# Kernel optimization log

Measured on AMD Instinct MI355X. Metric: run time of the kernel, lower is better.

## Reference

```python
import jax, jax.numpy as jnp
import numpy as np

N_NODES = 50000
N_EDGES = 1600000
IN_CH = 128
OUT_CH = 64
N_HEADS = 4


def setup_inputs() -> dict:
    key = jax.random.key(0)
    k1, k2, k3, k4, k5 = jax.random.split(key, 5)
    x_source = jax.random.normal(k1, (N_NODES, IN_CH), dtype=jnp.float32)
    edge_tgt = jax.random.randint(k2, (N_EDGES,), 0, N_NODES, dtype=jnp.int32)
    edge_src = jax.random.randint(k3, (N_EDGES,), 0, N_NODES, dtype=jnp.int32)
    edge_vals = jnp.ones((N_EDGES,), dtype=jnp.float32)
    # per-head learned params (xavier_uniform-ish scale)
    w_scale = float(np.sqrt(6.0 / (IN_CH + OUT_CH)))
    weight = jax.random.uniform(k4, (N_HEADS, IN_CH, OUT_CH), dtype=jnp.float32,
                                minval=-w_scale, maxval=w_scale)
    a_scale = float(np.sqrt(6.0 / (2 * OUT_CH)))
    att_weight = jax.random.uniform(k5, (N_HEADS, 2 * OUT_CH), dtype=jnp.float32,
                                    minval=-a_scale, maxval=a_scale)
    return {"x_source": x_source, "edge_tgt": edge_tgt, "edge_src": edge_src,
            "edge_vals": edge_vals, "weight": weight, "att_weight": att_weight}


def _can_forward(x_source, edge_tgt, edge_src, edge_vals, weight, att_weight):
    n_nodes = x_source.shape[0]
    out_ch = weight.shape[-1]
    # per-head linear transform: [N, H, O]
    x_msg = jnp.einsum('ni,hio->nho', x_source, weight)
    # gather per-edge source/target messages: [E, H, O]
    src_msg = x_msg[edge_src]
    tgt_msg = x_msg[edge_tgt]
    # attention score = cat([src, tgt]) @ att_weight, split halves: [E, H]
    aw_s = att_weight[:, :out_ch]
    aw_t = att_weight[:, out_ch:]
    e = jnp.einsum('eho,ho->eh', src_msg, aw_s) + jnp.einsum('eho,ho->eh', tgt_msg, aw_t)
    e = jax.nn.leaky_relu(e, negative_slope=0.01)  # default torch slope
    e = e * edge_vals[:, None]  # multiply by neighborhood values pre-softmax
    # sparse softmax over each target row (dim=1 of the sparse matrix)
    row_max = jax.ops.segment_max(e, edge_tgt, num_segments=n_nodes)  # [N, H]
    e_exp = jnp.exp(e - row_max[edge_tgt])
    row_sum = jax.ops.segment_sum(e_exp, edge_tgt, num_segments=n_nodes)  # [N, H]
    alpha = e_exp / row_sum[edge_tgt]  # [E, H]
    # weighted aggregate of source messages per target node: [N, H, O]
    out = jax.ops.segment_sum(alpha[:, :, None] * src_msg, edge_tgt,
                              num_segments=n_nodes)
    # concat heads -> [N, H*O]
    return out.reshape(n_nodes, -1)


def reference(x_source, edge_tgt, edge_src, edge_vals, weight, att_weight):
    return _can_forward(x_source, edge_tgt, edge_src, edge_vals, weight, att_weight)
```

## Files before the change

kernel.cpp:

```cpp
#include <hip/hip_runtime.h>
#include <hip/hip_bf16.h>
#include <math.h>

#define N_NODES 50000
#define N_EDGES 1600000
#define IN_CH   128
#define OUT_CH  64
#define N_HEADS 4
#define CH      (N_HEADS * OUT_CH)

#define NPB   64
#define BINS  782
#define CAPB  3072
#define CHUNK 8000

typedef __attribute__((ext_vector_type(8))) short bf16x8;
typedef __attribute__((ext_vector_type(4))) float f32x4;

__device__ __forceinline__ float bf16_lo(unsigned u) { return __uint_as_float(u << 16); }
__device__ __forceinline__ float bf16_hi(unsigned u) { return __uint_as_float(u & 0xffff0000u); }
__device__ __forceinline__ unsigned short f_to_bf16(float f) {
  unsigned u = __float_as_uint(f);
  u += 0x7fffu + ((u >> 16) & 1u);
  return (unsigned short)(u >> 16);
}

__global__ __launch_bounds__(256) void convert_w(
    const float* __restrict__ w, unsigned short* __restrict__ wb)
{
  int i = blockIdx.x * 256 + threadIdx.x;
  if (i >= N_HEADS * IN_CH * OUT_CH) return;
  int j = i & 7, lane = (i >> 3) & 63, ctg = (i >> 9) & 15, kc = i >> 13;
  int k = kc * 32 + (lane >> 4) * 8 + j;
  int n = ctg * 16 + (lane & 15);
  int h = n >> 6, o = n & 63;
  wb[i] = f_to_bf16(w[(h * IN_CH + k) * OUT_CH + o]);
}

__global__ __launch_bounds__(256) void init_cursors(int* __restrict__ gcur)
{
  int b = blockIdx.x * 256 + threadIdx.x;
  if (b < BINS) gcur[b] = b * CAPB;
}

__global__ __launch_bounds__(256) void gemm_mfma(
    const float* __restrict__ x, const unsigned short* __restrict__ wb,
    const float* __restrict__ aw,
    unsigned short* __restrict__ xmsg, float* __restrict__ sbuf, float* __restrict__ tbuf)
{
  __shared__ __align__(16) unsigned short tlds[4][32][128];

  const int lane = threadIdx.x & 63;
  const int wv   = threadIdx.x >> 6;
  const int q    = lane >> 4;
  const int l16  = lane & 15;
  const int rowbase = blockIdx.x * 64 + (wv >> 1) * 32;
  const int chalf   = wv & 1;

  bf16x8 afrag[2][4];
  #pragma unroll
  for (int s = 0; s < 2; ++s) {
    int r = rowbase + s * 16 + l16;
    r = min(r, N_NODES - 1);
    const float* xp = x + (size_t)r * IN_CH + q * 8;
    #pragma unroll
    for (int kc = 0; kc < 4; ++kc) {
      f32x4 lo = *(const f32x4*)(xp + kc * 32);
      f32x4 hi = *(const f32x4*)(xp + kc * 32 + 4);
      bf16x8 a;
      a[0] = (short)f_to_bf16(lo[0]); a[1] = (short)f_to_bf16(lo[1]);
      a[2] = (short)f_to_bf16(lo[2]); a[3] = (short)f_to_bf16(lo[3]);
      a[4] = (short)f_to_bf16(hi[0]); a[5] = (short)f_to_bf16(hi[1]);
      a[6] = (short)f_to_bf16(hi[2]); a[7] = (short)f_to_bf16(hi[3]);
      afrag[s][kc] = a;
    }
  }

  f32x4 acc[2][8];
  #pragma unroll
  for (int s = 0; s < 2; ++s)
    #pragma unroll
    for (int ct = 0; ct < 8; ++ct)
      acc[s][ct] = (f32x4){0.f, 0.f, 0.f, 0.f};

  #pragma unroll
  for (int kc = 0; kc < 4; ++kc) {
    #pragma unroll
    for (int ct = 0; ct < 8; ++ct) {
      const int ctg = chalf * 8 + ct;
      bf16x8 b = *(const bf16x8*)(wb + ((size_t)(kc * 16 + ctg) * 64 + lane) * 8);
      acc[0][ct] = __builtin_amdgcn_mfma_f32_16x16x32_bf16(afrag[0][kc], b, acc[0][ct], 0, 0, 0);
      acc[1][ct] = __builtin_amdgcn_mfma_f32_16x16x32_bf16(afrag[1][kc], b, acc[1][ct], 0, 0, 0);
    }
  }

  #pragma unroll
  for (int s = 0; s < 2; ++s)
    #pragma unroll
    for (int ct = 0; ct < 8; ++ct)
      #pragma unroll
      for (int reg = 0; reg < 4; ++reg)
        tlds[wv][s * 16 + q * 4 + reg][ct * 16 + l16] = f_to_bf16(acc[s][ct][reg]);

  #pragma unroll
  for (int s = 0; s < 2; ++s) {
    float ps[2][4] = {{0,0,0,0},{0,0,0,0}};
    float pt[2][4] = {{0,0,0,0},{0,0,0,0}};
    #pragma unroll
    for (int ct = 0; ct < 8; ++ct) {
      int col = chalf * 128 + ct * 16 + l16;
      int h = col >> 6;
      float as_ = aw[h * 128 + (col & 63)];
      float at_ = aw[h * 128 + 64 + (col & 63)];
      int hp = ct >> 2;
      #pragma unroll
      for (int reg = 0; reg < 4; ++reg) {
        float v = acc[s][ct][reg];
        ps[hp][reg] += v * as_;
        pt[hp][reg] += v * at_;
      }
    }
    #pragma unroll
    for (int hp = 0; hp < 2; ++hp)
      #pragma unroll
      for (int reg = 0; reg < 4; ++reg)
        #pragma unroll
        for (int off = 1; off < 16; off <<= 1) {
          ps[hp][reg] += __shfl_xor(ps[hp][reg], off);
          pt[hp][reg] += __shfl_xor(pt[hp][reg], off);
        }
    const int rowq = rowbase + s * 16 + q * 4;
    if (l16 == 0) {
      #pragma unroll
      for (int reg = 0; reg < 4; ++reg) {
        int r = rowq + reg;
        if (r < N_NODES) {
          #pragma unroll
          for (int hp = 0; hp < 2; ++hp) {
            sbuf[r * 4 + chalf * 2 + hp] = ps[hp][reg];
            tbuf[r * 4 + chalf * 2 + hp] = pt[hp][reg];
          }
        }
      }
    }
  }

  __syncthreads();

  const int seg  = lane & 31;
  const int half = lane >> 5;
  #pragma unroll
  for (int r2 = 0; r2 < 16; ++r2) {
    int row = r2 * 2 + half;
    int gr = rowbase + row;
    if (gr < N_NODES) {
      ushort4 vv = *(const ushort4*)&tlds[wv][row][seg * 4];
      *(ushort4*)(xmsg + (size_t)gr * CH + chalf * 128 + seg * 4) = vv;
    }
  }
}

__global__ __launch_bounds__(256) void bin_scatter(
    const int* __restrict__ etgt, const int* __restrict__ esrc,
    const float* __restrict__ eval, int* __restrict__ gcur, int2* __restrict__ binned)
{
  __shared__ int lhist[BINS];
  __shared__ int lbase[BINS];
  __shared__ unsigned short stg[CHUNK];

  const int tid = threadIdx.x;
  const int e0 = blockIdx.x * CHUNK;
  const int n = min(CHUNK, N_EDGES - e0);

  for (int b = tid; b < BINS; b += 256) lhist[b] = 0;
  __syncthreads();

  for (int i = tid; i < n; i += 256) {
    int t = etgt[e0 + i];
    stg[i] = (unsigned short)t;
    atomicAdd(&lhist[t >> 6], 1);
  }
  __syncthreads();

  for (int b = tid; b < BINS; b += 256) {
    int c = lhist[b];
    lbase[b] = c ? atomicAdd(&gcur[b], c) : 0;
    lhist[b] = 0;
  }
  __syncthreads();

  for (int i = tid; i < n; i += 256) {
    int t = (int)stg[i];
    int b = t >> 6;
    int r = atomicAdd(&lhist[b], 1);
    int pos = lbase[b] + r;
    if (pos < (b + 1) * CAPB) {
      int pack = esrc[e0 + i] | ((t & 63) << 16);
      binned[pos] = make_int2(pack, __float_as_int(eval[e0 + i]));
    }
  }
}

__global__ __launch_bounds__(256) void build_csr(
    const int* __restrict__ gcur, const int2* __restrict__ binned,
    int2* __restrict__ csr, int* __restrict__ deg, int* __restrict__ rowstart)
{
  __shared__ int nh[NPB];
  __shared__ int npre[NPB];
  __shared__ __align__(16) int2 stg[CAPB];

  const int tid = threadIdx.x;
  const int b = blockIdx.x;
  const int base = b * CAPB;
  const int cnt = min(gcur[b] - base, CAPB);

  if (tid < NPB) nh[tid] = 0;
  __syncthreads();

  for (int i = tid; i < cnt; i += 256) {
    int2 e = binned[base + i];
    stg[i] = e;
    atomicAdd(&nh[(e.x >> 16) & 63], 1);
  }
  __syncthreads();

  if (tid < 64) {
    int v = nh[tid];
    int sc = v;
    #pragma unroll
    for (int off = 1; off < 64; off <<= 1) {
      int u = __shfl_up(sc, off);
      if (tid >= off) sc += u;
    }
    npre[tid] = sc - v;
    int node = b * NPB + tid;
    if (node < N_NODES) { deg[node] = v; rowstart[node] = base + sc - v; }
    nh[tid] = 0;
  }
  __syncthreads();

  for (int i = tid; i < cnt; i += 256) {
    int2 e = stg[i];
    int tl = (e.x >> 16) & 63;
    int r = atomicAdd(&nh[tl], 1);
    csr[base + npre[tl] + r] = e;
  }
}

__global__ __launch_bounds__(256) void aggregate_kernel(
    const int* __restrict__ deg, const int* __restrict__ rowstart,
    const int2* __restrict__ csr,
    const float* __restrict__ sbuf, const float* __restrict__ tbuf,
    const unsigned short* __restrict__ xmsg, float* __restrict__ out)
{
  const int lane = threadIdx.x & 63;
  const int wave = threadIdx.x >> 6;
  const int n = blockIdx.x * 4 + wave;
  if (n >= N_NODES) return;

  __shared__ __align__(16) float p_lds[4][64][4];
  __shared__ int s_lds[4][64];

  const int d = deg[n];
  const int rs0 = rowstart[n];
  const int seg  = lane & 31;
  const int half = lane >> 5;
  const int hh4  = seg >> 3;

  float4 tn4 = *(const float4*)(tbuf + (size_t)n * 4);
  float tn[4] = {tn4.x, tn4.y, tn4.z, tn4.w};

  float m[4]    = {-INFINITY, -INFINITY, -INFINITY, -INFINITY};
  float psum[4] = {0.f, 0.f, 0.f, 0.f};
  float acc[8]  = {0.f, 0.f, 0.f, 0.f, 0.f, 0.f, 0.f, 0.f};

  for (int base = 0; base < d; base += 64) {
    const int cnt = min(64, d - base);
    const bool act = lane < cnt;

    float sc[4] = {-INFINITY, -INFINITY, -INFINITY, -INFINITY};
    int s = 0;
    if (act) {
      int2 ev = csr[(size_t)rs0 + base + lane];
      s = ev.x & 0xffff;
      float v = __int_as_float(ev.y);
      float4 sv4 = *(const float4*)(sbuf + (size_t)s * 4);
      float svv[4] = {sv4.x, sv4.y, sv4.z, sv4.w};
      #pragma unroll
      for (int hh = 0; hh < 4; ++hh) {
        float t = svv[hh] + tn[hh];
        t = (t > 0.f) ? t : 0.01f * t;
        sc[hh] = t * v;
      }
    }

    float bm[4] = {sc[0], sc[1], sc[2], sc[3]};
    #pragma unroll
    for (int hh = 0; hh < 4; ++hh)
      #pragma unroll
      for (int off = 32; off; off >>= 1)
        bm[hh] = fmaxf(bm[hh], __shfl_xor(bm[hh], off));

    float p[4];
    #pragma unroll
    for (int hh = 0; hh < 4; ++hh) {
      float nm = fmaxf(m[hh], bm[hh]);
      float r = (m[hh] == -INFINITY) ? 0.f : __expf(m[hh] - nm);
      psum[hh] *= r;
      if (hh == hh4) {
        #pragma unroll
        for (int j = 0; j < 8; ++j) acc[j] *= r;
      }
      m[hh] = nm;
      p[hh] = act ? __expf(sc[hh] - nm) : 0.f;
      psum[hh] += p[hh];
    }

    if (act) {
      s_lds[wave][lane] = s;
      *(float4*)(&p_lds[wave][lane][0]) = make_float4(p[0], p[1], p[2], p[3]);
    }
    __builtin_amdgcn_wave_barrier();

    int k = 0;
    for (; k + 8 <= cnt; k += 8) {
      int sA = s_lds[wave][k + 0 + half];
      int sB = s_lds[wave][k + 2 + half];
      int sC = s_lds[wave][k + 4 + half];
      int sD = s_lds[wave][k + 6 + half];
      uint4 rA = *(const uint4*)(xmsg + (size_t)sA * CH + seg * 8);
      uint4 rB = *(const uint4*)(xmsg + (size_t)sB * CH + seg * 8);
      uint4 rC = *(const uint4*)(xmsg + (size_t)sC * CH + seg * 8);
      uint4 rD = *(const uint4*)(xmsg + (size_t)sD * CH + seg * 8);
      float qA = p_lds[wave][k + 0 + half][hh4];
      float qB = p_lds[wave][k + 2 + half][hh4];
      float qC = p_lds[wave][k + 4 + half][hh4];
      float qD = p_lds[wave][k + 6 + half][hh4];
      acc[0] = fmaf(qA, bf16_lo(rA.x), acc[0]); acc[1] = fmaf(qA, bf16_hi(rA.x), acc[1]);
      acc[2] = fmaf(qA, bf16_lo(rA.y), acc[2]); acc[3] = fmaf(qA, bf16_hi(rA.y), acc[3]);
      acc[4] = fmaf(qA, bf16_lo(rA.z), acc[4]); acc[5] = fmaf(qA, bf16_hi(rA.z), acc[5]);
      acc[6] = fmaf(qA, bf16_lo(rA.w), acc[6]); acc[7] = fmaf(qA, bf16_hi(rA.w), acc[7]);
      acc[0] = fmaf(qB, bf16_lo(rB.x), acc[0]); acc[1] = fmaf(qB, bf16_hi(rB.x), acc[1]);
      acc[2] = fmaf(qB, bf16_lo(rB.y), acc[2]); acc[3] = fmaf(qB, bf16_hi(rB.y), acc[3]);
      acc[4] = fmaf(qB, bf16_lo(rB.z), acc[4]); acc[5] = fmaf(qB, bf16_hi(rB.z), acc[5]);
      acc[6] = fmaf(qB, bf16_lo(rB.w), acc[6]); acc[7] = fmaf(qB, bf16_hi(rB.w), acc[7]);
      acc[0] = fmaf(qC, bf16_lo(rC.x), acc[0]); acc[1] = fmaf(qC, bf16_hi(rC.x), acc[1]);
      acc[2] = fmaf(qC, bf16_lo(rC.y), acc[2]); acc[3] = fmaf(qC, bf16_hi(rC.y), acc[3]);
      acc[4] = fmaf(qC, bf16_lo(rC.z), acc[4]); acc[5] = fmaf(qC, bf16_hi(rC.z), acc[5]);
      acc[6] = fmaf(qC, bf16_lo(rC.w), acc[6]); acc[7] = fmaf(qC, bf16_hi(rC.w), acc[7]);
      acc[0] = fmaf(qD, bf16_lo(rD.x), acc[0]); acc[1] = fmaf(qD, bf16_hi(rD.x), acc[1]);
      acc[2] = fmaf(qD, bf16_lo(rD.y), acc[2]); acc[3] = fmaf(qD, bf16_hi(rD.y), acc[3]);
      acc[4] = fmaf(qD, bf16_lo(rD.z), acc[4]); acc[5] = fmaf(qD, bf16_hi(rD.z), acc[5]);
      acc[6] = fmaf(qD, bf16_lo(rD.w), acc[6]); acc[7] = fmaf(qD, bf16_hi(rD.w), acc[7]);
    }
    for (; k < cnt; k += 2) {
      int e = k + half;
      if (e < cnt) {
        int sA = s_lds[wave][e];
        uint4 rA = *(const uint4*)(xmsg + (size_t)sA * CH + seg * 8);
        float qA = p_lds[wave][e][hh4];
        acc[0] = fmaf(qA, bf16_lo(rA.x), acc[0]); acc[1] = fmaf(qA, bf16_hi(rA.x), acc[1]);
        acc[2] = fmaf(qA, bf16_lo(rA.y), acc[2]); acc[3] = fmaf(qA, bf16_hi(rA.y), acc[3]);
        acc[4] = fmaf(qA, bf16_lo(rA.z), acc[4]); acc[5] = fmaf(qA, bf16_hi(rA.z), acc[5]);
        acc[6] = fmaf(qA, bf16_lo(rA.w), acc[6]); acc[7] = fmaf(qA, bf16_hi(rA.w), acc[7]);
      }
    }
    __builtin_amdgcn_wave_barrier();
  }

  #pragma unroll
  for (int j = 0; j < 8; ++j) acc[j] += __shfl_xor(acc[j], 32);
  #pragma unroll
  for (int hh = 0; hh < 4; ++hh)
    #pragma unroll
    for (int off = 32; off; off >>= 1)
      psum[hh] += __shfl_xor(psum[hh], off);

  float rs = psum[hh4];
  float inv = (rs > 0.f) ? 1.0f / rs : 0.f;
  const int o = half * 4;
  float4 o4 = make_float4(acc[o+0]*inv, acc[o+1]*inv, acc[o+2]*inv, acc[o+3]*inv);
  *(float4*)(out + (size_t)n * CH + seg * 8 + half * 4) = o4;
}

extern "C" void kernel_launch(void* const* d_in, const int* in_sizes, int n_in,
                              void* d_out, int out_size, void* d_ws, size_t ws_size,
                              hipStream_t stream) {
  const float* x    = (const float*)d_in[0];
  const int*   etgt = (const int*)  d_in[1];
  const int*   esrc = (const int*)  d_in[2];
  const float* evl  = (const float*)d_in[3];
  const float* w    = (const float*)d_in[4];
  const float* aw   = (const float*)d_in[5];
  float* out = (float*)d_out;

  char* ws = (char*)d_ws;
  unsigned short* wb   = (unsigned short*)(ws);
  unsigned short* xmsg = (unsigned short*)(ws + 65536);
  float* sbuf     = (float*)(ws + 25665536);
  float* tbuf     = (float*)(ws + 26465536);
  int*   gcur     = (int*)  (ws + 27265536);
  int*   deg      = (int*)  (ws + 27269632);
  int*   rowstart = (int*)  (ws + 27470336);
  int2*  binned   = (int2*) (ws + 27671040);
  int2*  csr      = (int2*) (ws + 46889472);

  init_cursors<<<4, 256, 0, stream>>>(gcur);
  convert_w<<<128, 256, 0, stream>>>(w, wb);
  gemm_mfma<<<(N_NODES + 63) / 64, 256, 0, stream>>>(x, wb, aw, xmsg, sbuf, tbuf);
  bin_scatter<<<(N_EDGES + CHUNK - 1) / CHUNK, 256, 0, stream>>>(etgt, esrc, evl, gcur, binned);
  build_csr<<<BINS, 256, 0, stream>>>(gcur, binned, csr, deg, rowstart);
  aggregate_kernel<<<(N_NODES + 3) / 4, 256, 0, stream>>>(deg, rowstart, csr,
                                                          sbuf, tbuf, xmsg, out);
}
```

Baseline: 288.5 us.

## Merge prep kernels, transpose GEMM tiling, and aggregate two nodes per wave

Merges weight conversion and cursor init into one prep kernel. Swaps the MFMA operand roles so each wave computes all 256 output channels for 32 nodes, which removes the LDS transpose staging and the 16-lane shuffle reductions. The aggregation kernel now handles two target nodes per wave, interleaving their gathers to expose more memory-level parallelism. In exchange it uses more registers, may lower occupancy, and leaves work imbalanced when the two nodes have different degrees.

```diff
diff --git a/kernel.cpp b/kernel.cpp
--- a/kernel.cpp
+++ b/kernel.cpp
@@ -25,137 +25,103 @@
   return (unsigned short)(u >> 16);
 }
 
-__global__ __launch_bounds__(256) void convert_w(
-    const float* __restrict__ w, unsigned short* __restrict__ wb)
+__global__ __launch_bounds__(256) void prep_kernel(
+    const float* __restrict__ w, unsigned short* __restrict__ wb2,
+    int* __restrict__ gcur)
 {
-  int i = blockIdx.x * 256 + threadIdx.x;
-  if (i >= N_HEADS * IN_CH * OUT_CH) return;
-  int j = i & 7, lane = (i >> 3) & 63, ctg = (i >> 9) & 15, kc = i >> 13;
-  int k = kc * 32 + (lane >> 4) * 8 + j;
-  int n = ctg * 16 + (lane & 15);
-  int h = n >> 6, o = n & 63;
-  wb[i] = f_to_bf16(w[(h * IN_CH + k) * OUT_CH + o]);
-}
-
-__global__ __launch_bounds__(256) void init_cursors(int* __restrict__ gcur)
-{
-  int b = blockIdx.x * 256 + threadIdx.x;
-  if (b < BINS) gcur[b] = b * CAPB;
+  if (blockIdx.x < 128) {
+    int i = blockIdx.x * 256 + threadIdx.x;
+    int j = i & 7, lane = (i >> 3) & 63, kc = (i >> 9) & 3, mb = i >> 11;
+    int k = kc * 32 + (lane >> 4) * 8 + j;
+    int ch = mb * 16 + (lane & 15);
+    int h = ch >> 6, o = ch & 63;
+    wb2[i] = f_to_bf16(w[(h * IN_CH + k) * OUT_CH + o]);
+  } else {
+    for (int b = threadIdx.x; b < BINS; b += 256) gcur[b] = b * CAPB;
+  }
 }
 
 __global__ __launch_bounds__(256) void gemm_mfma(
-    const float* __restrict__ x, const unsigned short* __restrict__ wb,
+    const float* __restrict__ x, const unsigned short* __restrict__ wb2,
     const float* __restrict__ aw,
     unsigned short* __restrict__ xmsg, float* __restrict__ sbuf, float* __restrict__ tbuf)
 {
-  __shared__ __align__(16) unsigned short tlds[4][32][128];
-
   const int lane = threadIdx.x & 63;
   const int wv   = threadIdx.x >> 6;
   const int q    = lane >> 4;
   const int l16  = lane & 15;
-  const int rowbase = blockIdx.x * 64 + (wv >> 1) * 32;
-  const int chalf   = wv & 1;
-
-  bf16x8 afrag[2][4];
-  #pragma unroll
-  for (int s = 0; s < 2; ++s) {
-    int r = rowbase + s * 16 + l16;
-    r = min(r, N_NODES - 1);
-    const float* xp = x + (size_t)r * IN_CH + q * 8;
+  const int nb   = blockIdx.x * 128 + wv * 32;
+
+  bf16x8 bfrag[2][4];
+  #pragma unroll
+  for (int t = 0; t < 2; ++t) {
+    int node = min(nb + t * 16 + l16, N_NODES - 1);
+    const float* xp = x + (size_t)node * IN_CH + q * 8;
     #pragma unroll
     for (int kc = 0; kc < 4; ++kc) {
       f32x4 lo = *(const f32x4*)(xp + kc * 32);
       f32x4 hi = *(const f32x4*)(xp + kc * 32 + 4);
-      bf16x8 a;
-      a[0] = (short)f_to_bf16(lo[0]); a[1] = (short)f_to_bf16(lo[1]);
-      a[2] = (short)f_to_bf16(lo[2]); a[3] = (short)f_to_bf16(lo[3]);
-      a[4] = (short)f_to_bf16(hi[0]); a[5] = (short)f_to_bf16(hi[1]);
-      a[6] = (short)f_to_bf16(hi[2]); a[7] = (short)f_to_bf16(hi[3]);
-      afrag[s][kc] = a;
-    }
-  }
-
-  f32x4 acc[2][8];
-  #pragma unroll
-  for (int s = 0; s < 2; ++s)
-    #pragma unroll
-    for (int ct = 0; ct < 8; ++ct)
-      acc[s][ct] = (f32x4){0.f, 0.f, 0.f, 0.f};
+      bf16x8 b;
+      b[0] = (short)f_to_bf16(lo[0]); b[1] = (short)f_to_bf16(lo[1]);
+      b[2] = (short)f_to_bf16(lo[2]); b[3] = (short)f_to_bf16(lo[3]);
+      b[4] = (short)f_to_bf16(hi[0]); b[5] = (short)f_to_bf16(hi[1]);
+      b[6] = (short)f_to_bf16(hi[2]); b[7] = (short)f_to_bf16(hi[3]);
+      bfrag[t][kc] = b;
+    }
+  }
+
+  f32x4 acc[2][16];
+  #pragma unroll
+  for (int t = 0; t < 2; ++t)
+    #pragma unroll
+    for (int mb = 0; mb < 16; ++mb)
+      acc[t][mb] = (f32x4){0.f, 0.f, 0.f, 0.f};
 
   #pragma unroll
   for (int kc = 0; kc < 4; ++kc) {
     #pragma unroll
-    for (int ct = 0; ct < 8; ++ct) {
-      const int ctg = chalf * 8 + ct;
-      bf16x8 b = *(const bf16x8*)(wb + ((size_t)(kc * 16 + ctg) * 64 + lane) * 8);
-      acc[0][ct] = __builtin_amdgcn_mfma_f32_16x16x32_bf16(afrag[0][kc], b, acc[0][ct], 0, 0, 0);
-      acc[1][ct] = __builtin_amdgcn_mfma_f32_16x16x32_bf16(afrag[1][kc], b, acc[1][ct], 0, 0, 0);
-    }
-  }
-
-  #pragma unroll
-  for (int s = 0; s < 2; ++s)
-    #pragma unroll
-    for (int ct = 0; ct < 8; ++ct)
-      #pragma unroll
-      for (int reg = 0; reg < 4; ++reg)
-        tlds[wv][s * 16 + q * 4 + reg][ct * 16 + l16] = f_to_bf16(acc[s][ct][reg]);
-
-  #pragma unroll
-  for (int s = 0; s < 2; ++s) {
-    float ps[2][4] = {{0,0,0,0},{0,0,0,0}};
-    float pt[2][4] = {{0,0,0,0},{0,0,0,0}};
-    #pragma unroll
-    for (int ct = 0; ct < 8; ++ct) {
-      int col = chalf * 128 + ct * 16 + l16;
-      int h = col >> 6;
-      float as_ = aw[h * 128 + (col & 63)];
-      float at_ = aw[h * 128 + 64 + (col & 63)];
-      int hp = ct >> 2;
+    for (int mb = 0; mb < 16; ++mb) {
+      bf16x8 a = *(const bf16x8*)(wb2 + ((size_t)(mb * 4 + kc) * 64 + lane) * 8);
+      acc[0][mb] = __builtin_amdgcn_mfma_f32_16x16x32_bf16(a, bfrag[0][kc], acc[0][mb], 0, 0, 0);
+      acc[1][mb] = __builtin_amdgcn_mfma_f32_16x16x32_bf16(a, bfrag[1][kc], acc[1][mb], 0, 0, 0);
+    }
+  }
+
+  #pragma unroll
+  for (int t = 0; t < 2; ++t) {
+    const int node = nb + t * 16 + l16;
+    const bool valid = node < N_NODES;
+
+    float sv[4] = {0.f, 0.f, 0.f, 0.f};
+    float tv[4] = {0.f, 0.f, 0.f, 0.f};
+    #pragma unroll
+    for (int mb = 0; mb < 16; ++mb) {
+      ushort4 pk;
+      pk.x = f_to_bf16(acc[t][mb][0]); pk.y = f_to_bf16(acc[t][mb][1]);
+      pk.z = f_to_bf16(acc[t][mb][2]); pk.w = f_to_bf16(acc[t][mb][3]);
+      if (valid)
+        *(ushort4*)(xmsg + (size_t)node * CH + mb * 16 + q * 4) = pk;
+
+      const int h = mb >> 2;
+      const int o = (mb & 3) * 16 + q * 4;
       #pragma unroll
       for (int reg = 0; reg < 4; ++reg) {
-        float v = acc[s][ct][reg];
-        ps[hp][reg] += v * as_;
-        pt[hp][reg] += v * at_;
-      }
-    }
-    #pragma unroll
-    for (int hp = 0; hp < 2; ++hp)
-      #pragma unroll
-      for (int reg = 0; reg < 4; ++reg)
-        #pragma unroll
-        for (int off = 1; off < 16; off <<= 1) {
-          ps[hp][reg] += __shfl_xor(ps[hp][reg], off);
-          pt[hp][reg] += __shfl_xor(pt[hp][reg], off);
-        }
-    const int rowq = rowbase + s * 16 + q * 4;
-    if (l16 == 0) {
-      #pragma unroll
-      for (int reg = 0; reg < 4; ++reg) {
-        int r = rowq + reg;
-        if (r < N_NODES) {
-          #pragma unroll
-          for (int hp = 0; hp < 2; ++hp) {
-            sbuf[r * 4 + chalf * 2 + hp] = ps[hp][reg];
-            tbuf[r * 4 + chalf * 2 + hp] = pt[hp][reg];
-          }
-        }
-      }
-    }
-  }
-
-  __syncthreads();
-
-  const int seg  = lane & 31;
-  const int half = lane >> 5;
-  #pragma unroll
-  for (int r2 = 0; r2 < 16; ++r2) {
-    int row = r2 * 2 + half;
-    int gr = rowbase + row;
-    if (gr < N_NODES) {
-      ushort4 vv = *(const ushort4*)&tlds[wv][row][seg * 4];
-      *(ushort4*)(xmsg + (size_t)gr * CH + chalf * 128 + seg * 4) = vv;
+        float as_ = aw[h * 128 + o + reg];
+        float at_ = aw[h * 128 + 64 + o + reg];
+        sv[h] += acc[t][mb][reg] * as_;
+        tv[h] += acc[t][mb][reg] * at_;
+      }
+    }
+    #pragma unroll
+    for (int hh = 0; hh < 4; ++hh) {
+      sv[hh] += __shfl_xor(sv[hh], 16); sv[hh] += __shfl_xor(sv[hh], 32);
+      tv[hh] += __shfl_xor(tv[hh], 16); tv[hh] += __shfl_xor(tv[hh], 32);
+    }
+    float svq = (q == 0) ? sv[0] : (q == 1) ? sv[1] : (q == 2) ? sv[2] : sv[3];
+    float tvq = (q == 0) ? tv[0] : (q == 1) ? tv[1] : (q == 2) ? tv[2] : tv[3];
+    if (valid) {
+      sbuf[node * 4 + q] = svq;
+      tbuf[node * 4 + q] = tvq;
     }
   }
 }
@@ -255,132 +221,196 @@
 {
   const int lane = threadIdx.x & 63;
   const int wave = threadIdx.x >> 6;
-  const int n = blockIdx.x * 4 + wave;
-  if (n >= N_NODES) return;
-
-  __shared__ __align__(16) float p_lds[4][64][4];
-  __shared__ int s_lds[4][64];
-
-  const int d = deg[n];
-  const int rs0 = rowstart[n];
+  const int n0 = (blockIdx.x * 4 + wave) * 2;
+  const int n1 = n0 + 1;
+
+  __shared__ __align__(16) float p_lds[4][2][64][4];
+  __shared__ int s_lds[4][2][64];
+
   const int seg  = lane & 31;
   const int half = lane >> 5;
   const int hh4  = seg >> 3;
 
-  float4 tn4 = *(const float4*)(tbuf + (size_t)n * 4);
-  float tn[4] = {tn4.x, tn4.y, tn4.z, tn4.w};
-
-  float m[4]    = {-INFINITY, -INFINITY, -INFINITY, -INFINITY};
-  float psum[4] = {0.f, 0.f, 0.f, 0.f};
-  float acc[8]  = {0.f, 0.f, 0.f, 0.f, 0.f, 0.f, 0.f, 0.f};
-
-  for (int base = 0; base < d; base += 64) {
-    const int cnt = min(64, d - base);
-    const bool act = lane < cnt;
-
-    float sc[4] = {-INFINITY, -INFINITY, -INFINITY, -INFINITY};
-    int s = 0;
-    if (act) {
-      int2 ev = csr[(size_t)rs0 + base + lane];
-      s = ev.x & 0xffff;
-      float v = __int_as_float(ev.y);
-      float4 sv4 = *(const float4*)(sbuf + (size_t)s * 4);
-      float svv[4] = {sv4.x, sv4.y, sv4.z, sv4.w};
+  const int d0 = deg[n0], r0 = rowstart[n0];
+  const int d1 = deg[n1], r1 = rowstart[n1];
+
+  float4 t04 = *(const float4*)(tbuf + (size_t)n0 * 4);
+  float4 t14 = *(const float4*)(tbuf + (size_t)n1 * 4);
+  float tn0[4] = {t04.x, t04.y, t04.z, t04.w};
+  float tn1[4] = {t14.x, t14.y, t14.z, t14.w};
+
+  float m0[4] = {-INFINITY, -INFINITY, -INFINITY, -INFINITY};
+  float m1[4] = {-INFINITY, -INFINITY, -INFINITY, -INFINITY};
+  float ps0[4] = {0.f, 0.f, 0.f, 0.f};
+  float ps1[4] = {0.f, 0.f, 0.f, 0.f};
+  float acc0[8] = {0.f, 0.f, 0.f, 0.f, 0.f, 0.f, 0.f, 0.f};
+  float acc1[8] = {0.f, 0.f, 0.f, 0.f, 0.f, 0.f, 0.f, 0.f};
+
+  const int dmax = max(d0, d1);
+  for (int base = 0; base < dmax; base += 64) {
+    const int cnt0 = min(64, d0 - base);
+    const int cnt1 = min(64, d1 - base);
+    const bool any0 = cnt0 > 0, any1 = cnt1 > 0;
+    const bool act0 = lane < cnt0, act1 = lane < cnt1;
+
+    int2 ev0, ev1;
+    if (act0) ev0 = csr[(size_t)r0 + base + lane];
+    if (act1) ev1 = csr[(size_t)r1 + base + lane];
+    int s0 = 0, s1 = 0;
+    float4 sv40, sv41;
+    if (act0) { s0 = ev0.x & 0xffff; sv40 = *(const float4*)(sbuf + (size_t)s0 * 4); }
+    if (act1) { s1 = ev1.x & 0xffff; sv41 = *(const float4*)(sbuf + (size_t)s1 * 4); }
+
+    float sc0[4] = {-INFINITY, -INFINITY, -INFINITY, -INFINITY};
+    float sc1[4] = {-INFINITY, -INFINITY, -INFINITY, -INFINITY};
+    if (act0) {
+      float v = __int_as_float(ev0.y);
+      float sw[4] = {sv40.x, sv40.y, sv40.z, sv40.w};
       #pragma unroll
       for (int hh = 0; hh < 4; ++hh) {
-        float t = svv[hh] + tn[hh];
+        float t = sw[hh] + tn0[hh];
         t = (t > 0.f) ? t : 0.01f * t;
-        sc[hh] = t * v;
-      }
-    }
-
-    float bm[4] = {sc[0], sc[1], sc[2], sc[3]};
+        sc0[hh] = t * v;
+      }
+    }
+    if (act1) {
+      float v = __int_as_float(ev1.y);
+      float sw[4] = {sv41.x, sv41.y, sv41.z, sv41.w};
+      #pragma unroll
+      for (int hh = 0; hh < 4; ++hh) {
+        float t = sw[hh] + tn1[hh];
+        t = (t > 0.f) ? t : 0.01f * t;
+        sc1[hh] = t * v;
+      }
+    }
+
+    float bm0[4] = {sc0[0], sc0[1], sc0[2], sc0[3]};
+    float bm1[4] = {sc1[0], sc1[1], sc1[2], sc1[3]};
     #pragma unroll
     for (int hh = 0; hh < 4; ++hh)
       #pragma unroll
-      for (int off = 32; off; off >>= 1)
-        bm[hh] = fmaxf(bm[hh], __shfl_xor(bm[hh], off));
-
-    float p[4];
-    #pragma unroll
-    for (int hh = 0; hh < 4; ++hh) {
-      float nm = fmaxf(m[hh], bm[hh]);
-      float r = (m[hh] == -INFINITY) ? 0.f : __expf(m[hh] - nm);
-      psum[hh] *= r;
-      if (hh == hh4) {
+      for (int off = 32; off; off >>= 1) {
+        bm0[hh] = fmaxf(bm0[hh], __shfl_xor(bm0[hh], off));
+        bm1[hh] = fmaxf(bm1[hh], __shfl_xor(bm1[hh], off));
+      }
+
+    if (any0) {
+      float p[4];
+      #pragma unroll
+      for (int hh = 0; hh < 4; ++hh) {
+        float nm = fmaxf(m0[hh], bm0[hh]);
+        float r = (m0[hh] == -INFINITY) ? 0.f : __expf(m0[hh] - nm);
+        ps0[hh] *= r;
+        if (hh == hh4) {
+          #pragma unroll
+          for (int j = 0; j < 8; ++j) acc0[j] *= r;
+        }
+        m0[hh] = nm;
+        p[hh] = act0 ? __expf(sc0[hh] - nm) : 0.f;
+        ps0[hh] += p[hh];
+      }
+      if (act0) {
+        s_lds[wave][0][lane] = s0;
+        *(float4*)(&p_lds[wave][0][lane][0]) = make_float4(p[0], p[1], p[2], p[3]);
+      }
+    }
+    if (any1) {
+      float p[4];
+      #pragma unroll
+      for (int hh = 0; hh < 4; ++hh) {
+        float nm = fmaxf(m1[hh], bm1[hh]);
+        float r = (m1[hh] == -INFINITY) ? 0.f : __expf(m1[hh] - nm);
+        ps1[hh] *= r;
+        if (hh == hh4) {
+          #pragma unroll
+          for (int j = 0; j < 8; ++j) acc1[j] *= r;
+        }
+        m1[hh] = nm;
+        p[hh] = act1 ? __expf(sc1[hh] - nm) : 0.f;
+        ps1[hh] += p[hh];
+      }
+      if (act1) {
+        s_lds[wave][1][lane] = s1;
+        *(float4*)(&p_lds[wave][1][lane][0]) = make_float4(p[0], p[1], p[2], p[3]);
+      }
+    }
+    __builtin_amdgcn_wave_barrier();
+
+    const int kmax = max(max(cnt0, cnt1), 0);
+    for (int k = 0; k < kmax; k += 8) {
+      const bool g0 = k < cnt0, g1 = k < cnt1;
+      uint4 R0[4], R1[4];
+      float Q0[4], Q1[4];
+      if (g0) {
+        const int c = cnt0 - 1;
         #pragma unroll
-        for (int j = 0; j < 8; ++j) acc[j] *= r;
-      }
-      m[hh] = nm;
-      p[hh] = act ? __expf(sc[hh] - nm) : 0.f;
-      psum[hh] += p[hh];
-    }
-
-    if (act) {
-      s_lds[wave][lane] = s;
-      *(float4*)(&p_lds[wave][lane][0]) = make_float4(p[0], p[1], p[2], p[3]);
+        for (int i = 0; i < 4; ++i) {
+          int ii = k + 2 * i + half;
+          int j = min(ii, c);
+          R0[i] = *(const uint4*)(xmsg + (size_t)s_lds[wave][0][j] * CH + seg * 8);
+          Q0[i] = (ii < cnt0) ? p_lds[wave][0][j][hh4] : 0.f;
+        }
+      }
+      if (g1) {
+        const int c = cnt1 - 1;
+        #pragma unroll
+        for (int i = 0; i < 4; ++i) {
+          int ii = k + 2 * i + half;
+          int j = min(ii, c);
+          R1[i] = *(const uint4*)(xmsg + (size_t)s_lds[wave][1][j] * CH + seg * 8);
+          Q1[i] = (ii < cnt1) ? p_lds[wave][1][j][hh4] : 0.f;
+        }
+      }
+      if (g0) {
+        #pragma unroll
+        for (int i = 0; i < 4; ++i) {
+          float qq = Q0[i]; uint4 rr = R0[i];
+          acc0[0] = fmaf(qq, bf16_lo(rr.x), acc0[0]); acc0[1] = fmaf(qq, bf16_hi(rr.x), acc0[1]);
+          acc0[2] = fmaf(qq, bf16_lo(rr.y), acc0[2]); acc0[3] = fmaf(qq, bf16_hi(rr.y), acc0[3]);
+          acc0[4] = fmaf(qq, bf16_lo(rr.z), acc0[4]); acc0[5] = fmaf(qq, bf16_hi(rr.z), acc0[5]);
+          acc0[6] = fmaf(qq, bf16_lo(rr.w), acc0[6]); acc0[7] = fmaf(qq, bf16_hi(rr.w), acc0[7]);
+        }
+      }
+      if (g1) {
+        #pragma unroll
+        for (int i = 0; i < 4; ++i) {
+          float qq = Q1[i]; uint4 rr = R1[i];
+          acc1[0] = fmaf(qq, bf16_lo(rr.x), acc1[0]); acc1[1] = fmaf(qq, bf16_hi(rr.x), acc1[1]);
+          acc1[2] = fmaf(qq, bf16_lo(rr.y), acc1[2]); acc1[3] = fmaf(qq, bf16_hi(rr.y), acc1[3]);
+          acc1[4] = fmaf(qq, bf16_lo(rr.z), acc1[4]); acc1[5] = fmaf(qq, bf16_hi(rr.z), acc1[5]);
+          acc1[6] = fmaf(qq, bf16_lo(rr.w), acc1[6]); acc1[7] = fmaf(qq, bf16_hi(rr.w), acc1[7]);
+        }
+      }
     }
     __builtin_amdgcn_wave_barrier();
-
-    int k = 0;
-    for (; k + 8 <= cnt; k += 8) {
-      int sA = s_lds[wave][k + 0 + half];
-      int sB = s_lds[wave][k + 2 + half];
-      int sC = s_lds[wave][k + 4 + half];
-      int sD = s_lds[wave][k + 6 + half];
-      uint4 rA = *(const uint4*)(xmsg + (size_t)sA * CH + seg * 8);
-      uint4 rB = *(const uint4*)(xmsg + (size_t)sB * CH + seg * 8);
-      uint4 rC = *(const uint4*)(xmsg + (size_t)sC * CH + seg * 8);
-      uint4 rD = *(const uint4*)(xmsg + (size_t)sD * CH + seg * 8);
-      float qA = p_lds[wave][k + 0 + half][hh4];
-      float qB = p_lds[wave][k + 2 + half][hh4];
-      float qC = p_lds[wave][k + 4 + half][hh4];
-      float qD = p_lds[wave][k + 6 + half][hh4];
-      acc[0] = fmaf(qA, bf16_lo(rA.x), acc[0]); acc[1] = fmaf(qA, bf16_hi(rA.x), acc[1]);
-      acc[2] = fmaf(qA, bf16_lo(rA.y), acc[2]); acc[3] = fmaf(qA, bf16_hi(rA.y), acc[3]);
-      acc[4] = fmaf(qA, bf16_lo(rA.z), acc[4]); acc[5] = fmaf(qA, bf16_hi(rA.z), acc[5]);
-      acc[6] = fmaf(qA, bf16_lo(rA.w), acc[6]); acc[7] = fmaf(qA, bf16_hi(rA.w), acc[7]);
-      acc[0] = fmaf(qB, bf16_lo(rB.x), acc[0]); acc[1] = fmaf(qB, bf16_hi(rB.x), acc[1]);
-      acc[2] = fmaf(qB, bf16_lo(rB.y), acc[2]); acc[3] = fmaf(qB, bf16_hi(rB.y), acc[3]);
-      acc[4] = fmaf(qB, bf16_lo(rB.z), acc[4]); acc[5] = fmaf(qB, bf16_hi(rB.z), acc[5]);
-      acc[6] = fmaf(qB, bf16_lo(rB.w), acc[6]); acc[7] = fmaf(qB, bf16_hi(rB.w), acc[7]);
-      acc[0] = fmaf(qC, bf16_lo(rC.x), acc[0]); acc[1] = fmaf(qC, bf16_hi(rC.x), acc[1]);
-      acc[2] = fmaf(qC, bf16_lo(rC.y), acc[2]); acc[3] = fmaf(qC, bf16_hi(rC.y), acc[3]);
-      acc[4] = fmaf(qC, bf16_lo(rC.z), acc[4]); acc[5] = fmaf(qC, bf16_hi(rC.z), acc[5]);
-      acc[6] = fmaf(qC, bf16_lo(rC.w), acc[6]); acc[7] = fmaf(qC, bf16_hi(rC.w), acc[7]);
-      acc[0] = fmaf(qD, bf16_lo(rD.x), acc[0]); acc[1] = fmaf(qD, bf16_hi(rD.x), acc[1]);
-      acc[2] = fmaf(qD, bf16_lo(rD.y), acc[2]); acc[3] = fmaf(qD, bf16_hi(rD.y), acc[3]);
-      acc[4] = fmaf(qD, bf16_lo(rD.z), acc[4]); acc[5] = fmaf(qD, bf16_hi(rD.z), acc[5]);
-      acc[6] = fmaf(qD, bf16_lo(rD.w), acc[6]); acc[7] = fmaf(qD, bf16_hi(rD.w), acc[7]);
-    }
-    for (; k < cnt; k += 2) {
-      int e = k + half;
-      if (e < cnt) {
-        int sA = s_lds[wave][e];
-        uint4 rA = *(const uint4*)(xmsg + (size_t)sA * CH + seg * 8);
-        float qA = p_lds[wave][e][hh4];
-        acc[0] = fmaf(qA, bf16_lo(rA.x), acc[0]); acc[1] = fmaf(qA, bf16_hi(rA.x), acc[1]);
-        acc[2] = fmaf(qA, bf16_lo(rA.y), acc[2]); acc[3] = fmaf(qA, bf16_hi(rA.y), acc[3]);
-        acc[4] = fmaf(qA, bf16_lo(rA.z), acc[4]); acc[5] = fmaf(qA, bf16_hi(rA.z), acc[5]);
-        acc[6] = fmaf(qA, bf16_lo(rA.w), acc[6]); acc[7] = fmaf(qA, bf16_hi(rA.w), acc[7]);
-      }
-    }
-    __builtin_amdgcn_wave_barrier();
-  }
-
-  #pragma unroll
-  for (int j = 0; j < 8; ++j) acc[j] += __shfl_xor(acc[j], 32);
+  }
+
+  #pragma unroll
+  for (int j = 0; j < 8; ++j) {
+    acc0[j] += __shfl_xor(acc0[j], 32);
+    acc1[j] += __shfl_xor(acc1[j], 32);
+  }
   #pragma unroll
   for (int hh = 0; hh < 4; ++hh)
     #pragma unroll
-    for (int off = 32; off; off >>= 1)
-      psum[hh] += __shfl_xor(psum[hh], off);
-
-  float rs = psum[hh4];
-  float inv = (rs > 0.f) ? 1.0f / rs : 0.f;
+    for (int off = 32; off; off >>= 1) {
+      ps0[hh] += __shfl_xor(ps0[hh], off);
+      ps1[hh] += __shfl_xor(ps1[hh], off);
+    }
+
   const int o = half * 4;
-  float4 o4 = make_float4(acc[o+0]*inv, acc[o+1]*inv, acc[o+2]*inv, acc[o+3]*inv);
-  *(float4*)(out + (size_t)n * CH + seg * 8 + half * 4) = o4;
+  {
+    float rs = ps0[hh4];
+    float inv = (rs > 0.f) ? 1.0f / rs : 0.f;
+    float4 o4 = make_float4(acc0[o+0]*inv, acc0[o+1]*inv, acc0[o+2]*inv, acc0[o+3]*inv);
+    *(float4*)(out + (size_t)n0 * CH + seg * 8 + o) = o4;
+  }
+  {
+    float rs = ps1[hh4];
+    float inv = (rs > 0.f) ? 1.0f / rs : 0.f;
+    float4 o4 = make_float4(acc1[o+0]*inv, acc1[o+1]*inv, acc1[o+2]*inv, acc1[o+3]*inv);
+    *(float4*)(out + (size_t)n1 * CH + seg * 8 + o) = o4;
+  }
 }
 
 extern "C" void kernel_launch(void* const* d_in, const int* in_sizes, int n_in,
@@ -395,7 +425,7 @@
   float* out = (float*)d_out;
 
   char* ws = (char*)d_ws;
-  unsigned short* wb   = (unsigned short*)(ws);
+  unsigned short* wb2  = (unsigned short*)(ws);
   unsigned short* xmsg = (unsigned short*)(ws + 65536);
   float* sbuf     = (float*)(ws + 25665536);
   float* tbuf     = (float*)(ws + 26465536);
@@ -405,11 +435,10 @@
   int2*  binned   = (int2*) (ws + 27671040);
   int2*  csr      = (int2*) (ws + 46889472);
 
-  init_cursors<<<4, 256, 0, stream>>>(gcur);
-  convert_w<<<128, 256, 0, stream>>>(w, wb);
-  gemm_mfma<<<(N_NODES + 63) / 64, 256, 0, stream>>>(x, wb, aw, xmsg, sbuf, tbuf);
+  prep_kernel<<<129, 256, 0, stream>>>(w, wb2, gcur);
+  gemm_mfma<<<(N_NODES + 127) / 128, 256, 0, stream>>>(x, wb2, aw, xmsg, sbuf, tbuf);
   bin_scatter<<<(N_EDGES + CHUNK - 1) / CHUNK, 256, 0, stream>>>(etgt, esrc, evl, gcur, binned);
   build_csr<<<BINS, 256, 0, stream>>>(gcur, binned, csr, deg, rowstart);
-  aggregate_kernel<<<(N_NODES + 3) / 4, 256, 0, stream>>>(deg, rowstart, csr,
-                                                          sbuf, tbuf, xmsg, out);
-}
+  aggregate_kernel<<<N_NODES / 8, 256, 0, stream>>>(deg, rowstart, csr,
+                                                    sbuf, tbuf, xmsg, out);
+}
```

Result: no change. 293.5 us (+1.7%).

## Switch messages to fp16, use packed half FMA aggregation, restructure GEMM, merge prep kernels

Applied to the files above, without the earlier changes.

Stores the transformed messages in fp16 instead of bf16 and accumulates the weighted aggregation with packed half2 FMAs, which roughly halves the FMA count in the gather loop. The GEMM is rewritten with a transposed MFMA layout: each wave covers 32 nodes across all 256 channels and writes xmsg directly without the LDS staging buffer or block sync. The weight conversion and cursor init kernels are merged into one launch, and the bin_scatter chunk size is halved to launch more blocks. Accumulating in half precision risks precision loss and overflow on high-degree nodes.

```diff
diff --git a/kernel.cpp b/kernel.cpp
--- a/kernel.cpp
+++ b/kernel.cpp
@@ -1,5 +1,6 @@
 #include <hip/hip_runtime.h>
 #include <hip/hip_bf16.h>
+#include <hip/hip_fp16.h>
 #include <math.h>
 
 #define N_NODES 50000
@@ -12,150 +13,114 @@
 #define NPB   64
 #define BINS  782
 #define CAPB  3072
-#define CHUNK 8000
-
-typedef __attribute__((ext_vector_type(8))) short bf16x8;
+#define CHUNK 4000
+
+typedef __attribute__((ext_vector_type(8))) _Float16 f16x8;
 typedef __attribute__((ext_vector_type(4))) float f32x4;
 
-__device__ __forceinline__ float bf16_lo(unsigned u) { return __uint_as_float(u << 16); }
-__device__ __forceinline__ float bf16_hi(unsigned u) { return __uint_as_float(u & 0xffff0000u); }
-__device__ __forceinline__ unsigned short f_to_bf16(float f) {
-  unsigned u = __float_as_uint(f);
-  u += 0x7fffu + ((u >> 16) & 1u);
-  return (unsigned short)(u >> 16);
-}
-
-__global__ __launch_bounds__(256) void convert_w(
-    const float* __restrict__ w, unsigned short* __restrict__ wb)
-{
-  int i = blockIdx.x * 256 + threadIdx.x;
-  if (i >= N_HEADS * IN_CH * OUT_CH) return;
-  int j = i & 7, lane = (i >> 3) & 63, ctg = (i >> 9) & 15, kc = i >> 13;
-  int k = kc * 32 + (lane >> 4) * 8 + j;
-  int n = ctg * 16 + (lane & 15);
-  int h = n >> 6, o = n & 63;
-  wb[i] = f_to_bf16(w[(h * IN_CH + k) * OUT_CH + o]);
-}
-
-__global__ __launch_bounds__(256) void init_cursors(int* __restrict__ gcur)
-{
-  int b = blockIdx.x * 256 + threadIdx.x;
-  if (b < BINS) gcur[b] = b * CAPB;
+__device__ __forceinline__ __half2 u2h2(unsigned u) {
+  union { unsigned u; __half2 h; } c; c.u = u; return c.h;
+}
+
+__global__ __launch_bounds__(256) void prep_kernel(
+    const float* __restrict__ w, unsigned short* __restrict__ wb2,
+    int* __restrict__ gcur)
+{
+  if (blockIdx.x < 128) {
+    int i = blockIdx.x * 256 + threadIdx.x;
+    int j = i & 7, lane = (i >> 3) & 63, kc = (i >> 9) & 3, mb = i >> 11;
+    int k = kc * 32 + (lane >> 4) * 8 + j;
+    int ch = mb * 16 + (lane & 15);
+    int h = ch >> 6, o = ch & 63;
+    wb2[i] = __half_as_ushort(__float2half_rn(w[(h * IN_CH + k) * OUT_CH + o]));
+  } else {
+    for (int b = threadIdx.x; b < BINS; b += 256) gcur[b] = b * CAPB;
+  }
 }
 
 __global__ __launch_bounds__(256) void gemm_mfma(
-    const float* __restrict__ x, const unsigned short* __restrict__ wb,
+    const float* __restrict__ x, const unsigned short* __restrict__ wb2,
     const float* __restrict__ aw,
     unsigned short* __restrict__ xmsg, float* __restrict__ sbuf, float* __restrict__ tbuf)
 {
-  __shared__ __align__(16) unsigned short tlds[4][32][128];
-
   const int lane = threadIdx.x & 63;
   const int wv   = threadIdx.x >> 6;
   const int q    = lane >> 4;
   const int l16  = lane & 15;
-  const int rowbase = blockIdx.x * 64 + (wv >> 1) * 32;
-  const int chalf   = wv & 1;
-
-  bf16x8 afrag[2][4];
-  #pragma unroll
-  for (int s = 0; s < 2; ++s) {
-    int r = rowbase + s * 16 + l16;
-    r = min(r, N_NODES - 1);
-    const float* xp = x + (size_t)r * IN_CH + q * 8;
+  const int nb   = blockIdx.x * 128 + wv * 32;
+
+  f16x8 bfrag[2][4];
+  #pragma unroll
+  for (int t = 0; t < 2; ++t) {
+    int node = min(nb + t * 16 + l16, N_NODES - 1);
+    const float* xp = x + (size_t)node * IN_CH + q * 8;
     #pragma unroll
     for (int kc = 0; kc < 4; ++kc) {
       f32x4 lo = *(const f32x4*)(xp + kc * 32);
       f32x4 hi = *(const f32x4*)(xp + kc * 32 + 4);
-      bf16x8 a;
-      a[0] = (short)f_to_bf16(lo[0]); a[1] = (short)f_to_bf16(lo[1]);
-      a[2] = (short)f_to_bf16(lo[2]); a[3] = (short)f_to_bf16(lo[3]);
-      a[4] = (short)f_to_bf16(hi[0]); a[5] = (short)f_to_bf16(hi[1]);
-      a[6] = (short)f_to_bf16(hi[2]); a[7] = (short)f_to_bf16(hi[3]);
-      afrag[s][kc] = a;
-    }
-  }
-
-  f32x4 acc[2][8];
-  #pragma unroll
-  for (int s = 0; s < 2; ++s)
-    #pragma unroll
-    for (int ct = 0; ct < 8; ++ct)
-      acc[s][ct] = (f32x4){0.f, 0.f, 0.f, 0.f};
+      f16x8 b;
+      b[0] = (_Float16)lo[0]; b[1] = (_Float16)lo[1];
+      b[2] = (_Float16)lo[2]; b[3] = (_Float16)lo[3];
+      b[4] = (_Float16)hi[0]; b[5] = (_Float16)hi[1];
+      b[6] = (_Float16)hi[2]; b[7] = (_Float16)hi[3];
+      bfrag[t][kc] = b;
+    }
+  }
+
+  f32x4 acc[2][16];
+  #pragma unroll
+  for (int t = 0; t < 2; ++t)
+    #pragma unroll
+    for (int mb = 0; mb < 16; ++mb)
+      acc[t][mb] = (f32x4){0.f, 0.f, 0.f, 0.f};
 
   #pragma unroll
   for (int kc = 0; kc < 4; ++kc) {
     #pragma unroll
-    for (int ct = 0; ct < 8; ++ct) {
-      const int ctg = chalf * 8 + ct;
-      bf16x8 b = *(const bf16x8*)(wb + ((size_t)(kc * 16 + ctg) * 64 + lane) * 8);
-      acc[0][ct] = __builtin_amdgcn_mfma_f32_16x16x32_bf16(afrag[0][kc], b, acc[0][ct], 0, 0, 0);
-      acc[1][ct] = __builtin_amdgcn_mfma_f32_16x16x32_bf16(afrag[1][kc], b, acc[1][ct], 0, 0, 0);
-    }
-  }
-
-  #pragma unroll
-  for (int s = 0; s < 2; ++s)
-    #pragma unroll
-    for (int ct = 0; ct < 8; ++ct)
-      #pragma unroll
-      for (int reg = 0; reg < 4; ++reg)
-        tlds[wv][s * 16 + q * 4 + reg][ct * 16 + l16] = f_to_bf16(acc[s][ct][reg]);
-
-  #pragma unroll
-  for (int s = 0; s < 2; ++s) {
-    float ps[2][4] = {{0,0,0,0},{0,0,0,0}};
-    float pt[2][4] = {{0,0,0,0},{0,0,0,0}};
-    #pragma unroll
-    for (int ct = 0; ct < 8; ++ct) {
-      int col = chalf * 128 + ct * 16 + l16;
-      int h = col >> 6;
-      float as_ = aw[h * 128 + (col & 63)];
-      float at_ = aw[h * 128 + 64 + (col & 63)];
-      int hp = ct >> 2;
+    for (int mb = 0; mb < 16; ++mb) {
+      f16x8 a = *(const f16x8*)(wb2 + ((size_t)(mb * 4 + kc) * 64 + lane) * 8);
+      acc[0][mb] = __builtin_amdgcn_mfma_f32_16x16x32_f16(a, bfrag[0][kc], acc[0][mb], 0, 0, 0);
+      acc[1][mb] = __builtin_amdgcn_mfma_f32_16x16x32_f16(a, bfrag[1][kc], acc[1][mb], 0, 0, 0);
+    }
+  }
+
+  #pragma unroll
+  for (int t = 0; t < 2; ++t) {
+    const int node = nb + t * 16 + l16;
+    const bool valid = node < N_NODES;
+
+    float sv[4] = {0.f, 0.f, 0.f, 0.f};
+    float tv[4] = {0.f, 0.f, 0.f, 0.f};
+    #pragma unroll
+    for (int mb = 0; mb < 16; ++mb) {
+      ushort4 pk;
+      pk.x = __half_as_ushort(__float2half_rn(acc[t][mb][0]));
+      pk.y = __half_as_ushort(__float2half_rn(acc[t][mb][1]));
+      pk.z = __half_as_ushort(__float2half_rn(acc[t][mb][2]));
+      pk.w = __half_as_ushort(__float2half_rn(acc[t][mb][3]));
+      if (valid)
+        *(ushort4*)(xmsg + (size_t)node * CH + mb * 16 + q * 4) = pk;
+
+      const int h = mb >> 2;
+      const int o = (mb & 3) * 16 + q * 4;
       #pragma unroll
       for (int reg = 0; reg < 4; ++reg) {
-        float v = acc[s][ct][reg];
-        ps[hp][reg] += v * as_;
-        pt[hp][reg] += v * at_;
+        float as_ = aw[h * 128 + o + reg];
+        float at_ = aw[h * 128 + 64 + o + reg];
+        sv[h] += acc[t][mb][reg] * as_;
+        tv[h] += acc[t][mb][reg] * at_;
       }
     }
     #pragma unroll
-    for (int hp = 0; hp < 2; ++hp)
-      #pragma unroll
-      for (int reg = 0; reg < 4; ++reg)
-        #pragma unroll
-        for (int off = 1; off < 16; off <<= 1) {
-          ps[hp][reg] += __shfl_xor(ps[hp][reg], off);
-          pt[hp][reg] += __shfl_xor(pt[hp][reg], off);
-        }
-    const int rowq = rowbase + s * 16 + q * 4;
-    if (l16 == 0) {
-      #pragma unroll
-      for (int reg = 0; reg < 4; ++reg) {
-        int r = rowq + reg;
-        if (r < N_NODES) {
-          #pragma unroll
-          for (int hp = 0; hp < 2; ++hp) {
-            sbuf[r * 4 + chalf * 2 + hp] = ps[hp][reg];
-            tbuf[r * 4 + chalf * 2 + hp] = pt[hp][reg];
-          }
-        }
-      }
-    }
-  }
-
-  __syncthreads();
-
-  const int seg  = lane & 31;
-  const int half = lane >> 5;
-  #pragma unroll
-  for (int r2 = 0; r2 < 16; ++r2) {
-    int row = r2 * 2 + half;
-    int gr = rowbase + row;
-    if (gr < N_NODES) {
-      ushort4 vv = *(const ushort4*)&tlds[wv][row][seg * 4];
-      *(ushort4*)(xmsg + (size_t)gr * CH + chalf * 128 + seg * 4) = vv;
+    for (int hh = 0; hh < 4; ++hh) {
+      sv[hh] += __shfl_xor(sv[hh], 16); sv[hh] += __shfl_xor(sv[hh], 32);
+      tv[hh] += __shfl_xor(tv[hh], 16); tv[hh] += __shfl_xor(tv[hh], 32);
+    }
+    float svq = (q == 0) ? sv[0] : (q == 1) ? sv[1] : (q == 2) ? sv[2] : sv[3];
+    float tvq = (q == 0) ? tv[0] : (q == 1) ? tv[1] : (q == 2) ? tv[2] : tv[3];
+    if (valid) {
+      sbuf[node * 4 + q] = svq;
+      tbuf[node * 4 + q] = tvq;
     }
   }
 }
@@ -272,7 +237,9 @@
 
   float m[4]    = {-INFINITY, -INFINITY, -INFINITY, -INFINITY};
   float psum[4] = {0.f, 0.f, 0.f, 0.f};
-  float acc[8]  = {0.f, 0.f, 0.f, 0.f, 0.f, 0.f, 0.f, 0.f};
+  __half2 hacc[4];
+  #pragma unroll
+  for (int j = 0; j < 4; ++j) hacc[j] = __float2half2_rn(0.f);
 
   for (int base = 0; base < d; base += 64) {
     const int cnt = min(64, d - base);
@@ -308,8 +275,9 @@
       float r = (m[hh] == -INFINITY) ? 0.f : __expf(m[hh] - nm);
       psum[hh] *= r;
       if (hh == hh4) {
+        __half2 rh = __float2half2_rn(r);
         #pragma unroll
-        for (int j = 0; j < 8; ++j) acc[j] *= r;
+        for (int j = 0; j < 4; ++j) hacc[j] = __hmul2(hacc[j], rh);
       }
       m[hh] = nm;
       p[hh] = act ? __expf(sc[hh] - nm) : 0.f;
@@ -332,42 +300,48 @@
       uint4 rB = *(const uint4*)(xmsg + (size_t)sB * CH + seg * 8);
       uint4 rC = *(const uint4*)(xmsg + (size_t)sC * CH + seg * 8);
       uint4 rD = *(const uint4*)(xmsg + (size_t)sD * CH + seg * 8);
-      float qA = p_lds[wave][k + 0 + half][hh4];
-      float qB = p_lds[wave][k + 2 + half][hh4];
-      float qC = p_lds[wave][k + 4 + half][hh4];
-      float qD = p_lds[wave][k + 6 + half][hh4];
-      acc[0] = fmaf(qA, bf16_lo(rA.x), acc[0]); acc[1] = fmaf(qA, bf16_hi(rA.x), acc[1]);
-      acc[2] = fmaf(qA, bf16_lo(rA.y), acc[2]); acc[3] = fmaf(qA, bf16_hi(rA.y), acc[3]);
-      acc[4] = fmaf(qA, bf16_lo(rA.z), acc[4]); acc[5] = fmaf(qA, bf16_hi(rA.z), acc[5]);
-      acc[6] = fmaf(qA, bf16_lo(rA.w), acc[6]); acc[7] = fmaf(qA, bf16_hi(rA.w), acc[7]);
-      acc[0] = fmaf(qB, bf16_lo(rB.x), acc[0]); acc[1] = fmaf(qB, bf16_hi(rB.x), acc[1]);
-      acc[2] = fmaf(qB, bf16_lo(rB.y), acc[2]); acc[3] = fmaf(qB, bf16_hi(rB.y), acc[3]);
-      acc[4] = fmaf(qB, bf16_lo(rB.z), acc[4]); acc[5] = fmaf(qB, bf16_hi(rB.z), acc[5]);
-      acc[6] = fmaf(qB, bf16_lo(rB.w), acc[6]); acc[7] = fmaf(qB, bf16_hi(rB.w), acc[7]);
-      acc[0] = fmaf(qC, bf16_lo(rC.x), acc[0]); acc[1] = fmaf(qC, bf16_hi(rC.x), acc[1]);
-      acc[2] = fmaf(qC, bf16_lo(rC.y), acc[2]); acc[3] = fmaf(qC, bf16_hi(rC.y), acc[3]);
-      acc[4] = fmaf(qC, bf16_lo(rC.z), acc[4]); acc[5] = fmaf(qC, bf16_hi(rC.z), acc[5]);
-      acc[6] = fmaf(qC, bf16_lo(rC.w), acc[6]); acc[7] = fmaf(qC, bf16_hi(rC.w), acc[7]);
-      acc[0] = fmaf(qD, bf16_lo(rD.x), acc[0]); acc[1] = fmaf(qD, bf16_hi(rD.x), acc[1]);
-      acc[2] = fmaf(qD, bf16_lo(rD.y), acc[2]); acc[3] = fmaf(qD, bf16_hi(rD.y), acc[3]);
-      acc[4] = fmaf(qD, bf16_lo(rD.z), acc[4]); acc[5] = fmaf(qD, bf16_hi(rD.z), acc[5]);
-      acc[6] = fmaf(qD, bf16_lo(rD.w), acc[6]); acc[7] = fmaf(qD, bf16_hi(rD.w), acc[7]);
+      __half2 qA = __float2half2_rn(p_lds[wave][k + 0 + half][hh4]);
+      __half2 qB = __float2half2_rn(p_lds[wave][k + 2 + half][hh4]);
+      __half2 qC = __float2half2_rn(p_lds[wave][k + 4 + half][hh4]);
+      __half2 qD = __float2half2_rn(p_lds[wave][k + 6 + half][hh4]);
+      hacc[0] = __hfma2(qA, u2h2(rA.x), hacc[0]);
+      hacc[1] = __hfma2(qA, u2h2(rA.y), hacc[1]);
+      hacc[2] = __hfma2(qA, u2h2(rA.z), hacc[2]);
+      hacc[3] = __hfma2(qA, u2h2(rA.w), hacc[3]);
+      hacc[0] = __hfma2(qB, u2h2(rB.x), hacc[0]);
+      hacc[1] = __hfma2(qB, u2h2(rB.y), hacc[1]);
+      hacc[2] = __hfma2(qB, u2h2(rB.z), hacc[2]);
+      hacc[3] = __hfma2(qB, u2h2(rB.w), hacc[3]);
+      hacc[0] = __hfma2(qC, u2h2(rC.x), hacc[0]);
+      hacc[1] = __hfma2(qC, u2h2(rC.y), hacc[1]);
+      hacc[2] = __hfma2(qC, u2h2(rC.z), hacc[2]);
+      hacc[3] = __hfma2(qC, u2h2(rC.w), hacc[3]);
+      hacc[0] = __hfma2(qD, u2h2(rD.x), hacc[0]);
+      hacc[1] = __hfma2(qD, u2h2(rD.y), hacc[1]);
+      hacc[2] = __hfma2(qD, u2h2(rD.z), hacc[2]);
+      hacc[3] = __hfma2(qD, u2h2(rD.w), hacc[3]);
     }
     for (; k < cnt; k += 2) {
       int e = k + half;
       if (e < cnt) {
         int sA = s_lds[wave][e];
         uint4 rA = *(const uint4*)(xmsg + (size_t)sA * CH + seg * 8);
-        float qA = p_lds[wave][e][hh4];
-        acc[0] = fmaf(qA, bf16_lo(rA.x), acc[0]); acc[1] = fmaf(qA, bf16_hi(rA.x), acc[1]);
-        acc[2] = fmaf(qA, bf16_lo(rA.y), acc[2]); acc[3] = fmaf(qA, bf16_hi(rA.y), acc[3]);
-        acc[4] = fmaf(qA, bf16_lo(rA.z), acc[4]); acc[5] = fmaf(qA, bf16_hi(rA.z), acc[5]);
-        acc[6] = fmaf(qA, bf16_lo(rA.w), acc[6]); acc[7] = fmaf(qA, bf16_hi(rA.w), acc[7]);
+        __half2 qA = __float2half2_rn(p_lds[wave][e][hh4]);
+        hacc[0] = __hfma2(qA, u2h2(rA.x), hacc[0]);
+        hacc[1] = __hfma2(qA, u2h2(rA.y), hacc[1]);
+        hacc[2] = __hfma2(qA, u2h2(rA.z), hacc[2]);
+        hacc[3] = __hfma2(qA, u2h2(rA.w), hacc[3]);
       }
     }
     __builtin_amdgcn_wave_barrier();
   }
 
+  float acc[8];
+  #pragma unroll
+  for (int j = 0; j < 4; ++j) {
+    acc[2*j]   = __low2float(hacc[j]);
+    acc[2*j+1] = __high2float(hacc[j]);
+  }
   #pragma unroll
   for (int j = 0; j < 8; ++j) acc[j] += __shfl_xor(acc[j], 32);
   #pragma unroll
@@ -380,7 +354,7 @@
   float inv = (rs > 0.f) ? 1.0f / rs : 0.f;
   const int o = half * 4;
   float4 o4 = make_float4(acc[o+0]*inv, acc[o+1]*inv, acc[o+2]*inv, acc[o+3]*inv);
-  *(float4*)(out + (size_t)n * CH + seg * 8 + half * 4) = o4;
+  *(float4*)(out + (size_t)n * CH + seg * 8 + o) = o4;
 }
 
 extern "C" void kernel_launch(void* const* d_in, const int* in_sizes, int n_in,
@@ -395,7 +369,7 @@
   float* out = (float*)d_out;
 
   char* ws = (char*)d_ws;
-  unsigned short* wb   = (unsigned short*)(ws);
+  unsigned short* wb2  = (unsigned short*)(ws);
   unsigned short* xmsg = (unsigned short*)(ws + 65536);
   float* sbuf     = (float*)(ws + 25665536);
   float* tbuf     = (float*)(ws + 26465536);
@@ -405,9 +379,8 @@
   int2*  binned   = (int2*) (ws + 27671040);
   int2*  csr      = (int2*) (ws + 46889472);
 
-  init_cursors<<<4, 256, 0, stream>>>(gcur);
-  convert_w<<<128, 256, 0, stream>>>(w, wb);
-  gemm_mfma<<<(N_NODES + 63) / 64, 256, 0, stream>>>(x, wb, aw, xmsg, sbuf, tbuf);
+  prep_kernel<<<129, 256, 0, stream>>>(w, wb2, gcur);
+  gemm_mfma<<<(N_NODES + 127) / 128, 256, 0, stream>>>(x, wb2, aw, xmsg, sbuf, tbuf);
   bin_scatter<<<(N_EDGES + CHUNK - 1) / CHUNK, 256, 0, stream>>>(etgt, esrc, evl, gcur, binned);
   build_csr<<<BINS, 256, 0, stream>>>(gcur, binned, csr, deg, rowstart);
   aggregate_kernel<<<(N_NODES + 3) / 4, 256, 0, stream>>>(deg, rowstart, csr,
```

Result: no change. 291.8 us (+1.1%).
